# Kernel optimization log

Hardware: AMD Instinct MI355X
Metric: run time of the kernel (lower is better)

Reference implementation:

```python
import jax, jax.numpy as jnp
import numpy as np

SEQ_LEN = 64  # config.SEQ_LEN
T, B, N, D = 256, 128, 4, 2
H_HIS, H_INT = 32, 8


def _uniform(key, shape, k):
    return jax.random.uniform(key, shape, jnp.float32, -k, k)


def setup_inputs() -> dict:
    key = jax.random.key(0)
    ks = jax.random.split(key, 12)
    kh = 1.0 / np.sqrt(H_HIS)
    ki = 1.0 / np.sqrt(H_INT)
    ko = 1.0 / np.sqrt(40)
    return {
        "inputs": jax.random.normal(ks[0], (T, B, N, D), jnp.float32),
        # history LSTM (input 2 -> hidden 32), gate order i,f,g,o like torch
        "Wih_his": _uniform(ks[1], (4 * H_HIS, D), kh),
        "Whh_his": _uniform(ks[2], (4 * H_HIS, H_HIS), kh),
        "bih_his": _uniform(ks[3], (4 * H_HIS,), kh),
        "bhh_his": _uniform(ks[4], (4 * H_HIS,), kh),
        # interaction LSTM (input 2 -> hidden 8)
        "Wih_int": _uniform(ks[5], (4 * H_INT, D), ki),
        "Whh_int": _uniform(ks[6], (4 * H_INT, H_INT), ki),
        "bih_int": _uniform(ks[7], (4 * H_INT,), ki),
        "bhh_int": _uniform(ks[8], (4 * H_INT,), ki),
        # output Linear(40 -> 2)
        "W_out": _uniform(ks[9], (2, H_HIS + H_INT), ko),
        "b_out": _uniform(ks[10], (2,), ko),
    }


def _lstm_windows(x_w, valid, Wih, Whh, bih, bhh):
    """Run an LSTM over L steps for T independent windows at once.
    x_w: [L, Tw, B, d]  inputs per step (leading padding for short windows)
    valid: [L, Tw] bool; while False the state is held at zero, which is
    exactly equivalent to starting the window fresh at its first valid step.
    Returns final hidden state h: [Tw, B, H].
    """
    H = Whh.shape[1]
    Tw, Bb = x_w.shape[1], x_w.shape[2]
    b = bih + bhh

    def step(carry, xs):
        h, c = carry
        x, v = xs
        g = x @ Wih.T + h @ Whh.T + b            # [Tw, B, 4H]
        i, f, gg, o = jnp.split(g, 4, axis=-1)
        c_new = jax.nn.sigmoid(f) * c + jax.nn.sigmoid(i) * jnp.tanh(gg)
        h_new = jax.nn.sigmoid(o) * jnp.tanh(c_new)
        m = v[:, None, None]
        return (jnp.where(m, h_new, 0.0), jnp.where(m, c_new, 0.0)), None

    init = (jnp.zeros((Tw, Bb, H), x_w.dtype), jnp.zeros((Tw, Bb, H), x_w.dtype))
    (h, _), _ = jax.lax.scan(step, init, (x_w, valid))
    return h


def reference(inputs, Wih_his, Whh_his, bih_his, bhh_his,
              Wih_int, Whh_int, bih_int, bhh_int, W_out, b_out):
    Tt, Bb, Nn, Dd = inputs.shape
    L = SEQ_LEN
    # window index for output frame t: frames t-L+1 .. t (clipped; invalid masked)
    t = jnp.arange(Tt)[:, None]
    s = jnp.arange(L)[None, :]
    idx = t - (L - 1) + s                      # [T, L]
    valid = (idx >= 0)
    idx_c = jnp.clip(idx, 0, Tt - 1)
    x_his = inputs[:, :, -1, :][idx_c]         # [T, L, B, d] (ego / last node)
    x_int = inputs[:, :, 0, :][idx_c]          # [T, L, B, d] (interaction node)
    x_his = jnp.transpose(x_his, (1, 0, 2, 3))  # [L, T, B, d]
    x_int = jnp.transpose(x_int, (1, 0, 2, 3))
    v = jnp.transpose(valid)                   # [L, T]

    h_his = _lstm_windows(x_his, v, Wih_his, Whh_his, bih_his, bhh_his)  # [T,B,32]
    h_int = _lstm_windows(x_int, v, Wih_int, Whh_int, bih_int, bhh_int)  # [T,B,8]
    emb = jnp.concatenate([h_his, h_int], axis=-1)                       # [T,B,40]
    return emb @ W_out.T + b_out                                         # [T,B,2]
```

## Files before the change

kernel.cpp:

```cpp
#include <hip/hip_runtime.h>


typedef float v2f __attribute__((ext_vector_type(2)));
typedef float v4f __attribute__((ext_vector_type(4)));
typedef _Float16 h8v __attribute__((ext_vector_type(8)));

static __device__ __forceinline__ float fexp2(float x) {
    return __builtin_amdgcn_exp2f(x);
}
static __device__ __forceinline__ float frcp(float x) {
    return __builtin_amdgcn_rcpf(x);
}
static __device__ __forceinline__ void pk_fma(v2f& d, v2f a, v2f b) {
    asm("v_pk_fma_f32 %0, %1, %2, %0" : "+v"(d) : "v"(a), "v"(b));
}
static __device__ __forceinline__ v2f loh(v4f v) {
    return __builtin_shufflevector(v, v, 0, 1);
}
static __device__ __forceinline__ v2f hih(v4f v) {
    return __builtin_shufflevector(v, v, 2, 3);
}
static __device__ __forceinline__ unsigned short f2h(float f) {
    _Float16 h = (_Float16)f;
    unsigned short u;
    __builtin_memcpy(&u, &h, 2);
    return u;
}

#define LOG2E    1.442695041f
#define TWOLOG2E 2.885390082f

__global__ __launch_bounds__(256) void prep_kernel(
    const float* __restrict__ Wih_his, const float* __restrict__ Whh_his,
    const float* __restrict__ bih_his, const float* __restrict__ bhh_his,
    const float* __restrict__ Wih_int, const float* __restrict__ Whh_int,
    const float* __restrict__ bih_int, const float* __restrict__ bhh_int,
    float* __restrict__ ws)
{
    const int i = blockIdx.x * 256 + threadIdx.x;
    if (i < 4480) {
        if (i < 256) {
            const int r = i >> 1;
            const float s = (r >= 64 && r < 96) ? -TWOLOG2E : -LOG2E;
            ws[i] = Wih_his[i] * s;
        } else if (i < 384) {
            const int r = i - 256;
            const float s = (r >= 64 && r < 96) ? -TWOLOG2E : -LOG2E;
            ws[i] = (bih_his[r] + bhh_his[r]) * s;
        } else {
            const int e = i - 384, r = e >> 5;
            const float s = (r >= 64 && r < 96) ? -TWOLOG2E : -LOG2E;
            ws[i] = Whh_his[e] * s;
        }
    } else if (i < 4544) {
        const int e = i - 4480, r = e >> 1;
        const float s = (r >= 16 && r < 24) ? -TWOLOG2E : -LOG2E;
        ws[i] = Wih_int[e] * s;
    } else if (i < 4576) {
        const int r = i - 4544;
        const float s = (r >= 16 && r < 24) ? -TWOLOG2E : -LOG2E;
        ws[i] = (bih_int[r] + bhh_int[r]) * s;
    } else if (i < 4832) {
        const int e = i - 4576, r = e >> 3;
        const float s = (r >= 16 && r < 24) ? -TWOLOG2E : -LOG2E;
        ws[i] = Whh_int[e] * s;
    } else if (i < 4960) {
        const int p = i - 4832;
        const int T = p >> 4, n = p & 15;
        const int gi = T >> 1, u = 2 * n + (T & 1);
        const int r = gi * 32 + u;
        const float s = (gi == 2) ? -TWOLOG2E : -LOG2E;
        ws[5120 + p] = (bih_his[r] + bhh_his[r]) * s;
    } else if (i < 5216) {
        const int e = i - 4960;
        const int p = e >> 1, comp = e & 1;
        const int T = p >> 4, n = p & 15;
        const int gi = T >> 1, u = 2 * n + (T & 1);
        const int r = gi * 32 + u;
        const float s = (gi == 2) ? -TWOLOG2E : -LOG2E;
        ws[5376 + e] = Wih_his[r * 2 + comp] * s;
    } else if (i < 9312) {
        const int e = i - 5216;
        const int p = e >> 5, k = e & 31;
        const int T = p >> 4, n = p & 15;
        const int gi = T >> 1, u = 2 * n + (T & 1);
        const int r = gi * 32 + u;
        const float s = (gi == 2) ? -TWOLOG2E : -LOG2E;
        reinterpret_cast<unsigned short*>(ws)[11776 + e] =
            f2h(Whh_his[r * 32 + k] * s);
    }
}

__global__ __launch_bounds__(64) void int_kernel(
    const float* __restrict__ inp, const float* __restrict__ ws,
    const float* __restrict__ W_out, float* __restrict__ eInt)
{
    __shared__ __align__(16) float ib[2][8][8];

    const int lane = threadIdx.x;
    const int W    = blockIdx.x;
    const int t    = W >> 4;
    const int g    = lane >> 3;
    const int u    = lane & 7;
    const int b    = ((W & 15) << 3) | g;
    const int nsteps = (t >= 63) ? 64 : (t + 1);
    const int tau0   = (t >= 63) ? (t - 63) : 0;

    v2f wi[4][4], wxi[4];
    float bi[4];
    {
        const v2f* wsWi = reinterpret_cast<const v2f*>(ws + 4576);
        const v2f* wsXi = reinterpret_cast<const v2f*>(ws + 4480);
#pragma unroll
        for (int q = 0; q < 4; ++q) {
            const v2f* row = wsWi + (q * 8 + u) * 4;
#pragma unroll
            for (int k = 0; k < 4; ++k) wi[q][k] = row[k];
            bi[q]  = ws[4544 + q * 8 + u];
            wxi[q] = wsXi[q * 8 + u];
        }
    }

    ib[0][g][u] = 0.f;
    float cc = 0.f, h = 0.f;

    const float* xc = inp + tau0 * 1024 + b * 8;
    float2 xv2 = *reinterpret_cast<const float2*>(xc);
    xc += 1024;

#pragma unroll 1
    for (int s = 0; s < nsteps; ++s) {
        __builtin_amdgcn_wave_barrier();
        asm volatile("s_waitcnt lgkmcnt(0)" ::: "memory");
        __builtin_amdgcn_wave_barrier();

        const int rb = s & 1, wb = rb ^ 1;
        const v4f* ip = reinterpret_cast<const v4f*>(&ib[rb][g][0]);
        const v4f i0 = ip[0], i1 = ip[1];

        float2 nx = {0.f, 0.f};
        if (s + 1 < nsteps) nx = *reinterpret_cast<const float2*>(xc);
        xc += 1024;
        const v2f xv = {xv2.x, xv2.y};

        float a[4];
#pragma unroll
        for (int q = 0; q < 4; ++q) {
            v2f acc = {bi[q], 0.f};
            pk_fma(acc, wxi[q], xv);
            pk_fma(acc, wi[q][0], loh(i0));
            pk_fma(acc, wi[q][1], hih(i0));
            pk_fma(acc, wi[q][2], loh(i1));
            pk_fma(acc, wi[q][3], hih(i1));
            a[q] = acc.x + acc.y;
        }
        const float si = frcp(1.f + fexp2(a[0]));
        const float sf = frcp(1.f + fexp2(a[1]));
        const float tg = fmaf(2.f, frcp(1.f + fexp2(a[2])), -1.f);
        const float so = frcp(1.f + fexp2(a[3]));
        cc = fmaf(sf, cc, si * tg);
        h = so * fmaf(-2.f, frcp(1.f + fexp2(TWOLOG2E * cc)), 1.f);
        ib[wb][g][u] = h;

        xv2 = nx;
    }

    float e0 = W_out[32 + u] * h;
    float e1 = W_out[72 + u] * h;
#pragma unroll
    for (int m = 4; m >= 1; m >>= 1) {
        e0 += __shfl_xor(e0, m);
        e1 += __shfl_xor(e1, m);
    }
    if (u == 0) {
        float2 o; o.x = e0; o.y = e1;
        reinterpret_cast<float2*>(eInt)[t * 128 + b] = o;
    }
}

__global__ __launch_bounds__(64) void his_kernel(
    const float* __restrict__ inp, const float* __restrict__ ws,
    const float* __restrict__ W_out, const float* __restrict__ b_out,
    const float* __restrict__ eInt, float* __restrict__ out)
{
    __shared__ __align__(16) unsigned short hm[2][16][40];

    const int lane = threadIdx.x;
    const int n    = lane & 15;
    const int quad = lane >> 4;
    const int Wd   = blockIdx.x;
    const int t    = Wd >> 3;
    const int bg   = Wd & 7;
    const int nsteps = (t >= 63) ? 64 : (t + 1);
    const int tau0   = (t >= 63) ? (t - 63) : 0;

    h8v Bf[8];
    {
        const h8v* wb = reinterpret_cast<const h8v*>(
            reinterpret_cast<const unsigned short*>(ws) + 11776);
#pragma unroll
        for (int T = 0; T < 8; ++T) Bf[T] = wb[(T * 16 + n) * 4 + quad];
    }
    float cb[8], cw0[8], cw1[8];
#pragma unroll
    for (int T = 0; T < 8; ++T) {
        const int p = T * 16 + n;
        cb[T]  = ws[5120 + p];
        cw0[T] = ws[5376 + 2 * p];
        cw1[T] = ws[5376 + 2 * p + 1];
    }

    const int bbase = bg * 16 + quad * 4;
    const float* xp = inp + tau0 * 1024 + bbase * 8 + 6;
    float2 xc[4];
#pragma unroll
    for (int r = 0; r < 4; ++r)
        xc[r] = *reinterpret_cast<const float2*>(xp + r * 8);
    xp += 1024;

    h8v Af = {};
    float cs[4][2] = {};
    float h0[4] = {}, h1[4] = {};

#pragma unroll 1
    for (int s = 0; s < nsteps; ++s) {
        float2 xn[4];
        if (s + 1 < nsteps) {
#pragma unroll
            for (int r = 0; r < 4; ++r)
                xn[r] = *reinterpret_cast<const float2*>(xp + r * 8);
        } else {
#pragma unroll
            for (int r = 0; r < 4; ++r) xn[r] = make_float2(0.f, 0.f);
        }
        xp += 1024;

        v4f D[8];
#pragma unroll
        for (int T = 0; T < 8; ++T) {
            v4f C;
#pragma unroll
            for (int r = 0; r < 4; ++r)
                C[r] = fmaf(cw1[T], xc[r].y, fmaf(cw0[T], xc[r].x, cb[T]));
            D[T] = __builtin_amdgcn_mfma_f32_16x16x32_f16(Af, Bf[T], C, 0, 0, 0);
        }

#pragma unroll
        for (int r = 0; r < 4; ++r) {
            {
                const float si = frcp(1.f + fexp2(D[0][r]));
                const float sf = frcp(1.f + fexp2(D[2][r]));
                const float tg = fmaf(2.f, frcp(1.f + fexp2(D[4][r])), -1.f);
                const float so = frcp(1.f + fexp2(D[6][r]));
                const float cn = fmaf(sf, cs[r][0], si * tg);
                cs[r][0] = cn;
                h0[r] = so * fmaf(-2.f, frcp(1.f + fexp2(TWOLOG2E * cn)), 1.f);
            }
            {
                const float si = frcp(1.f + fexp2(D[1][r]));
                const float sf = frcp(1.f + fexp2(D[3][r]));
                const float tg = fmaf(2.f, frcp(1.f + fexp2(D[5][r])), -1.f);
                const float so = frcp(1.f + fexp2(D[7][r]));
                const float cn = fmaf(sf, cs[r][1], si * tg);
                cs[r][1] = cn;
                h1[r] = so * fmaf(-2.f, frcp(1.f + fexp2(TWOLOG2E * cn)), 1.f);
            }
        }

        if (s + 1 < nsteps) {
            const int bf = s & 1;
#pragma unroll
            for (int r = 0; r < 4; ++r) {
                const unsigned pk =
                    ((unsigned)f2h(h1[r]) << 16) | f2h(h0[r]);
                *reinterpret_cast<unsigned*>(&hm[bf][quad * 4 + r][2 * n]) = pk;
            }
            __builtin_amdgcn_wave_barrier();
            asm volatile("s_waitcnt lgkmcnt(0)" ::: "memory");
            __builtin_amdgcn_wave_barrier();
            Af = *reinterpret_cast<const h8v*>(&hm[bf][n][quad * 8]);
        }

#pragma unroll
        for (int r = 0; r < 4; ++r) xc[r] = xn[r];
    }

    const float wo0a = W_out[2 * n],      wo0b = W_out[2 * n + 1];
    const float wo1a = W_out[40 + 2 * n], wo1b = W_out[40 + 2 * n + 1];
    float e0[4], e1[4];
#pragma unroll
    for (int r = 0; r < 4; ++r) {
        e0[r] = fmaf(wo0b, h1[r], wo0a * h0[r]);
        e1[r] = fmaf(wo1b, h1[r], wo1a * h0[r]);
#pragma unroll
        for (int m = 1; m <= 8; m <<= 1) {
            e0[r] += __shfl_xor(e0[r], m);
            e1[r] += __shfl_xor(e1[r], m);
        }
    }
    if (n == 0) {
        const float bo0 = b_out[0], bo1 = b_out[1];
#pragma unroll
        for (int r = 0; r < 4; ++r) {
            const int chain = t * 128 + bbase + r;
            const float2 ei = reinterpret_cast<const float2*>(eInt)[chain];
            float2 o;
            o.x = e0[r] + ei.x + bo0;
            o.y = e1[r] + ei.y + bo1;
            reinterpret_cast<float2*>(out)[chain] = o;
        }
    }
}

extern "C" void kernel_launch(void* const* d_in, const int* in_sizes, int n_in,
                              void* d_out, int out_size, void* d_ws, size_t ws_size,
                              hipStream_t stream) {
    const float* inp     = (const float*)d_in[0];
    const float* Wih_his = (const float*)d_in[1];
    const float* Whh_his = (const float*)d_in[2];
    const float* bih_his = (const float*)d_in[3];
    const float* bhh_his = (const float*)d_in[4];
    const float* Wih_int = (const float*)d_in[5];
    const float* Whh_int = (const float*)d_in[6];
    const float* bih_int = (const float*)d_in[7];
    const float* bhh_int = (const float*)d_in[8];
    const float* W_out   = (const float*)d_in[9];
    const float* b_out   = (const float*)d_in[10];
    float* out  = (float*)d_out;
    float* ws   = (float*)d_ws;
    float* eInt = ws + 8192;

    prep_kernel<<<dim3(37), dim3(256), 0, stream>>>(
        Wih_his, Whh_his, bih_his, bhh_his,
        Wih_int, Whh_int, bih_int, bhh_int, ws);

    int_kernel<<<dim3(4096), dim3(64), 0, stream>>>(inp, ws, W_out, eInt);

    his_kernel<<<dim3(2048), dim3(64), 0, stream>>>(
        inp, ws, W_out, b_out, eInt, out);
}
```

Measured before the change: 209.8 us.

## Fuse interaction LSTM into history kernel using MFMA with padded weights

Removes the separate scalar interaction-LSTM kernel and its eInt intermediate, and computes the 8-unit interaction LSTM inside the history kernel. The interaction recurrence now uses two zero-padded 16x16x32 f16 MFMAs per step, with gate exchange done by lane shuffles. The prep kernel writes the reordered f16 interaction weights. This saves a kernel launch and the eInt round trip, and lets the two recurrences overlap in one wave. The cost is extra MFMA and transcendental work on the history kernel's critical path, plus f16 precision for the interaction recurrent weights.

```diff
diff --git a/kernel.cpp b/kernel.cpp
--- a/kernel.cpp
+++ b/kernel.cpp
@@ -1,7 +1,6 @@
 #include <hip/hip_runtime.h>
 
 
-typedef float v2f __attribute__((ext_vector_type(2)));
 typedef float v4f __attribute__((ext_vector_type(4)));
 typedef _Float16 h8v __attribute__((ext_vector_type(8)));
 
@@ -10,15 +9,6 @@
 }
 static __device__ __forceinline__ float frcp(float x) {
     return __builtin_amdgcn_rcpf(x);
-}
-static __device__ __forceinline__ void pk_fma(v2f& d, v2f a, v2f b) {
-    asm("v_pk_fma_f32 %0, %1, %2, %0" : "+v"(d) : "v"(a), "v"(b));
-}
-static __device__ __forceinline__ v2f loh(v4f v) {
-    return __builtin_shufflevector(v, v, 0, 1);
-}
-static __device__ __forceinline__ v2f hih(v4f v) {
-    return __builtin_shufflevector(v, v, 2, 3);
 }
 static __device__ __forceinline__ unsigned short f2h(float f) {
     _Float16 h = (_Float16)f;
@@ -38,152 +28,64 @@
     float* __restrict__ ws)
 {
     const int i = blockIdx.x * 256 + threadIdx.x;
-    if (i < 4480) {
-        if (i < 256) {
-            const int r = i >> 1;
-            const float s = (r >= 64 && r < 96) ? -TWOLOG2E : -LOG2E;
-            ws[i] = Wih_his[i] * s;
-        } else if (i < 384) {
-            const int r = i - 256;
-            const float s = (r >= 64 && r < 96) ? -TWOLOG2E : -LOG2E;
-            ws[i] = (bih_his[r] + bhh_his[r]) * s;
-        } else {
-            const int e = i - 384, r = e >> 5;
-            const float s = (r >= 64 && r < 96) ? -TWOLOG2E : -LOG2E;
-            ws[i] = Whh_his[e] * s;
-        }
-    } else if (i < 4544) {
-        const int e = i - 4480, r = e >> 1;
-        const float s = (r >= 16 && r < 24) ? -TWOLOG2E : -LOG2E;
-        ws[i] = Wih_int[e] * s;
-    } else if (i < 4576) {
-        const int r = i - 4544;
-        const float s = (r >= 16 && r < 24) ? -TWOLOG2E : -LOG2E;
-        ws[i] = (bih_int[r] + bhh_int[r]) * s;
-    } else if (i < 4832) {
-        const int e = i - 4576, r = e >> 3;
-        const float s = (r >= 16 && r < 24) ? -TWOLOG2E : -LOG2E;
-        ws[i] = Whh_int[e] * s;
-    } else if (i < 4960) {
-        const int p = i - 4832;
+    unsigned short* wsu = reinterpret_cast<unsigned short*>(ws);
+    if (i < 128) {
+        const int p = i;
         const int T = p >> 4, n = p & 15;
         const int gi = T >> 1, u = 2 * n + (T & 1);
         const int r = gi * 32 + u;
         const float s = (gi == 2) ? -TWOLOG2E : -LOG2E;
         ws[5120 + p] = (bih_his[r] + bhh_his[r]) * s;
-    } else if (i < 5216) {
-        const int e = i - 4960;
+    } else if (i < 384) {
+        const int e = i - 128;
         const int p = e >> 1, comp = e & 1;
         const int T = p >> 4, n = p & 15;
         const int gi = T >> 1, u = 2 * n + (T & 1);
         const int r = gi * 32 + u;
         const float s = (gi == 2) ? -TWOLOG2E : -LOG2E;
         ws[5376 + e] = Wih_his[r * 2 + comp] * s;
-    } else if (i < 9312) {
-        const int e = i - 5216;
+    } else if (i < 4480) {
+        const int e = i - 384;
         const int p = e >> 5, k = e & 31;
         const int T = p >> 4, n = p & 15;
         const int gi = T >> 1, u = 2 * n + (T & 1);
         const int r = gi * 32 + u;
         const float s = (gi == 2) ? -TWOLOG2E : -LOG2E;
-        reinterpret_cast<unsigned short*>(ws)[11776 + e] =
-            f2h(Whh_his[r * 32 + k] * s);
-    }
-}
-
-__global__ __launch_bounds__(64) void int_kernel(
-    const float* __restrict__ inp, const float* __restrict__ ws,
-    const float* __restrict__ W_out, float* __restrict__ eInt)
-{
-    __shared__ __align__(16) float ib[2][8][8];
-
-    const int lane = threadIdx.x;
-    const int W    = blockIdx.x;
-    const int t    = W >> 4;
-    const int g    = lane >> 3;
-    const int u    = lane & 7;
-    const int b    = ((W & 15) << 3) | g;
-    const int nsteps = (t >= 63) ? 64 : (t + 1);
-    const int tau0   = (t >= 63) ? (t - 63) : 0;
-
-    v2f wi[4][4], wxi[4];
-    float bi[4];
-    {
-        const v2f* wsWi = reinterpret_cast<const v2f*>(ws + 4576);
-        const v2f* wsXi = reinterpret_cast<const v2f*>(ws + 4480);
-#pragma unroll
-        for (int q = 0; q < 4; ++q) {
-            const v2f* row = wsWi + (q * 8 + u) * 4;
-#pragma unroll
-            for (int k = 0; k < 4; ++k) wi[q][k] = row[k];
-            bi[q]  = ws[4544 + q * 8 + u];
-            wxi[q] = wsXi[q * 8 + u];
-        }
-    }
-
-    ib[0][g][u] = 0.f;
-    float cc = 0.f, h = 0.f;
-
-    const float* xc = inp + tau0 * 1024 + b * 8;
-    float2 xv2 = *reinterpret_cast<const float2*>(xc);
-    xc += 1024;
-
-#pragma unroll 1
-    for (int s = 0; s < nsteps; ++s) {
-        __builtin_amdgcn_wave_barrier();
-        asm volatile("s_waitcnt lgkmcnt(0)" ::: "memory");
-        __builtin_amdgcn_wave_barrier();
-
-        const int rb = s & 1, wb = rb ^ 1;
-        const v4f* ip = reinterpret_cast<const v4f*>(&ib[rb][g][0]);
-        const v4f i0 = ip[0], i1 = ip[1];
-
-        float2 nx = {0.f, 0.f};
-        if (s + 1 < nsteps) nx = *reinterpret_cast<const float2*>(xc);
-        xc += 1024;
-        const v2f xv = {xv2.x, xv2.y};
-
-        float a[4];
-#pragma unroll
-        for (int q = 0; q < 4; ++q) {
-            v2f acc = {bi[q], 0.f};
-            pk_fma(acc, wxi[q], xv);
-            pk_fma(acc, wi[q][0], loh(i0));
-            pk_fma(acc, wi[q][1], hih(i0));
-            pk_fma(acc, wi[q][2], loh(i1));
-            pk_fma(acc, wi[q][3], hih(i1));
-            a[q] = acc.x + acc.y;
-        }
-        const float si = frcp(1.f + fexp2(a[0]));
-        const float sf = frcp(1.f + fexp2(a[1]));
-        const float tg = fmaf(2.f, frcp(1.f + fexp2(a[2])), -1.f);
-        const float so = frcp(1.f + fexp2(a[3]));
-        cc = fmaf(sf, cc, si * tg);
-        h = so * fmaf(-2.f, frcp(1.f + fexp2(TWOLOG2E * cc)), 1.f);
-        ib[wb][g][u] = h;
-
-        xv2 = nx;
-    }
-
-    float e0 = W_out[32 + u] * h;
-    float e1 = W_out[72 + u] * h;
-#pragma unroll
-    for (int m = 4; m >= 1; m >>= 1) {
-        e0 += __shfl_xor(e0, m);
-        e1 += __shfl_xor(e1, m);
-    }
-    if (u == 0) {
-        float2 o; o.x = e0; o.y = e1;
-        reinterpret_cast<float2*>(eInt)[t * 128 + b] = o;
-    }
-}
-
-__global__ __launch_bounds__(64) void his_kernel(
+        wsu[11776 + e] = f2h(Whh_his[r * 32 + k] * s);
+    } else if (i < 4512) {
+        const int p2 = i - 4480;
+        const int t = p2 >> 4, n = p2 & 15;
+        const int r2 = (t == 0) ? ((n < 8) ? n : n + 8)
+                                : ((n < 8) ? n + 8 : n + 16);
+        const float s = (r2 >= 16 && r2 < 24) ? -TWOLOG2E : -LOG2E;
+        ws[8192 + p2] = (bih_int[r2] + bhh_int[r2]) * s;
+    } else if (i < 4576) {
+        const int e = i - 4512;
+        const int p2 = e >> 1, comp = e & 1;
+        const int t = p2 >> 4, n = p2 & 15;
+        const int r2 = (t == 0) ? ((n < 8) ? n : n + 8)
+                                : ((n < 8) ? n + 8 : n + 16);
+        const float s = (r2 >= 16 && r2 < 24) ? -TWOLOG2E : -LOG2E;
+        ws[8224 + e] = Wih_int[r2 * 2 + comp] * s;
+    } else if (i < 5600) {
+        const int e = i - 4576;
+        const int p2 = e >> 5, k = e & 31;
+        const int t = p2 >> 4, n = p2 & 15;
+        const int r2 = (t == 0) ? ((n < 8) ? n : n + 8)
+                                : ((n < 8) ? n + 8 : n + 16);
+        const float s = (r2 >= 16 && r2 < 24) ? -TWOLOG2E : -LOG2E;
+        wsu[16640 + e] = (k < 8) ? f2h(Whh_int[r2 * 8 + k] * s)
+                                 : (unsigned short)0;
+    }
+}
+
+__global__ __launch_bounds__(64) void traj_kernel(
     const float* __restrict__ inp, const float* __restrict__ ws,
     const float* __restrict__ W_out, const float* __restrict__ b_out,
-    const float* __restrict__ eInt, float* __restrict__ out)
+    float* __restrict__ out)
 {
     __shared__ __align__(16) unsigned short hm[2][16][40];
+    __shared__ __align__(16) unsigned short hmI[2][16][8];
 
     const int lane = threadIdx.x;
     const int n    = lane & 15;
@@ -193,15 +95,20 @@
     const int bg   = Wd & 7;
     const int nsteps = (t >= 63) ? 64 : (t + 1);
     const int tau0   = (t >= 63) ? (t - 63) : 0;
-
-    h8v Bf[8];
+    const bool lo  = (n < 8);
+
+    h8v Bf[8], BfI[2];
     {
         const h8v* wb = reinterpret_cast<const h8v*>(
             reinterpret_cast<const unsigned short*>(ws) + 11776);
 #pragma unroll
         for (int T = 0; T < 8; ++T) Bf[T] = wb[(T * 16 + n) * 4 + quad];
-    }
-    float cb[8], cw0[8], cw1[8];
+        const h8v* wbI = reinterpret_cast<const h8v*>(
+            reinterpret_cast<const unsigned short*>(ws) + 16640);
+#pragma unroll
+        for (int T = 0; T < 2; ++T) BfI[T] = wbI[(T * 16 + n) * 4 + quad];
+    }
+    float cb[8], cw0[8], cw1[8], cbI[2], cwI0[2], cwI1[2];
 #pragma unroll
     for (int T = 0; T < 8; ++T) {
         const int p = T * 16 + n;
@@ -209,31 +116,45 @@
         cw0[T] = ws[5376 + 2 * p];
         cw1[T] = ws[5376 + 2 * p + 1];
     }
+#pragma unroll
+    for (int T = 0; T < 2; ++T) {
+        const int p2 = T * 16 + n;
+        cbI[T]  = ws[8192 + p2];
+        cwI0[T] = ws[8224 + 2 * p2];
+        cwI1[T] = ws[8224 + 2 * p2 + 1];
+    }
 
     const int bbase = bg * 16 + quad * 4;
-    const float* xp = inp + tau0 * 1024 + bbase * 8 + 6;
-    float2 xc[4];
-#pragma unroll
-    for (int r = 0; r < 4; ++r)
-        xc[r] = *reinterpret_cast<const float2*>(xp + r * 8);
-    xp += 1024;
-
-    h8v Af = {};
-    float cs[4][2] = {};
-    float h0[4] = {}, h1[4] = {};
+    const float* xpB = inp + tau0 * 1024 + bbase * 8;
+    float2 xc[4], xcI[4];
+#pragma unroll
+    for (int r = 0; r < 4; ++r) {
+        xc[r]  = *reinterpret_cast<const float2*>(xpB + r * 8 + 6);
+        xcI[r] = *reinterpret_cast<const float2*>(xpB + r * 8);
+    }
+    xpB += 1024;
+
+    h8v Af = {}, Afi = {};
+    float cs[4][2] = {}, csI[4] = {};
+    float h0[4] = {}, h1[4] = {}, hI[4] = {};
 
 #pragma unroll 1
     for (int s = 0; s < nsteps; ++s) {
-        float2 xn[4];
+        float2 xn[4], xnI[4];
         if (s + 1 < nsteps) {
 #pragma unroll
-            for (int r = 0; r < 4; ++r)
-                xn[r] = *reinterpret_cast<const float2*>(xp + r * 8);
+            for (int r = 0; r < 4; ++r) {
+                xn[r]  = *reinterpret_cast<const float2*>(xpB + r * 8 + 6);
+                xnI[r] = *reinterpret_cast<const float2*>(xpB + r * 8);
+            }
         } else {
 #pragma unroll
-            for (int r = 0; r < 4; ++r) xn[r] = make_float2(0.f, 0.f);
-        }
-        xp += 1024;
+            for (int r = 0; r < 4; ++r) {
+                xn[r] = make_float2(0.f, 0.f);
+                xnI[r] = make_float2(0.f, 0.f);
+            }
+        }
+        xpB += 1024;
 
         v4f D[8];
 #pragma unroll
@@ -243,6 +164,15 @@
             for (int r = 0; r < 4; ++r)
                 C[r] = fmaf(cw1[T], xc[r].y, fmaf(cw0[T], xc[r].x, cb[T]));
             D[T] = __builtin_amdgcn_mfma_f32_16x16x32_f16(Af, Bf[T], C, 0, 0, 0);
+        }
+        v4f DI[2];
+#pragma unroll
+        for (int T = 0; T < 2; ++T) {
+            v4f C;
+#pragma unroll
+            for (int r = 0; r < 4; ++r)
+                C[r] = fmaf(cwI1[T], xcI[r].y, fmaf(cwI0[T], xcI[r].x, cbI[T]));
+            DI[T] = __builtin_amdgcn_mfma_f32_16x16x32_f16(Afi, BfI[T], C, 0, 0, 0);
         }
 
 #pragma unroll
@@ -267,6 +197,22 @@
             }
         }
 
+#pragma unroll
+        for (int r = 0; r < 4; ++r) {
+            const float r0 = frcp(1.f + fexp2(DI[0][r]));
+            const float v0 = lo ? r0 : fmaf(2.f, r0, -1.f);
+            const float v1 = frcp(1.f + fexp2(DI[1][r]));
+            const float o0 = __shfl_xor(v0, 8);
+            const float o1 = __shfl_xor(v1, 8);
+            const float gi = lo ? v0 : o0;
+            const float gf = lo ? v1 : o1;
+            const float gg = lo ? o0 : v0;
+            const float go = lo ? o1 : v1;
+            const float cn = fmaf(gf, csI[r], gi * gg);
+            csI[r] = cn;
+            hI[r] = go * fmaf(-2.f, frcp(1.f + fexp2(TWOLOG2E * cn)), 1.f);
+        }
+
         if (s + 1 < nsteps) {
             const int bf = s & 1;
 #pragma unroll
@@ -275,14 +221,21 @@
                     ((unsigned)f2h(h1[r]) << 16) | f2h(h0[r]);
                 *reinterpret_cast<unsigned*>(&hm[bf][quad * 4 + r][2 * n]) = pk;
             }
+            if (lo) {
+#pragma unroll
+                for (int r = 0; r < 4; ++r)
+                    hmI[bf][quad * 4 + r][n] = f2h(hI[r]);
+            }
             __builtin_amdgcn_wave_barrier();
             asm volatile("s_waitcnt lgkmcnt(0)" ::: "memory");
             __builtin_amdgcn_wave_barrier();
             Af = *reinterpret_cast<const h8v*>(&hm[bf][n][quad * 8]);
-        }
-
-#pragma unroll
-        for (int r = 0; r < 4; ++r) xc[r] = xn[r];
+            if (quad == 0)
+                Afi = *reinterpret_cast<const h8v*>(&hmI[bf][n][0]);
+        }
+
+#pragma unroll
+        for (int r = 0; r < 4; ++r) { xc[r] = xn[r]; xcI[r] = xnI[r]; }
     }
 
     const float wo0a = W_out[2 * n],      wo0b = W_out[2 * n + 1];
@@ -292,6 +245,10 @@
     for (int r = 0; r < 4; ++r) {
         e0[r] = fmaf(wo0b, h1[r], wo0a * h0[r]);
         e1[r] = fmaf(wo1b, h1[r], wo1a * h0[r]);
+        if (lo) {
+            e0[r] = fmaf(W_out[32 + n], hI[r], e0[r]);
+            e1[r] = fmaf(W_out[72 + n], hI[r], e1[r]);
+        }
 #pragma unroll
         for (int m = 1; m <= 8; m <<= 1) {
             e0[r] += __shfl_xor(e0[r], m);
@@ -303,10 +260,9 @@
 #pragma unroll
         for (int r = 0; r < 4; ++r) {
             const int chain = t * 128 + bbase + r;
-            const float2 ei = reinterpret_cast<const float2*>(eInt)[chain];
             float2 o;
-            o.x = e0[r] + ei.x + bo0;
-            o.y = e1[r] + ei.y + bo1;
+            o.x = e0[r] + bo0;
+            o.y = e1[r] + bo1;
             reinterpret_cast<float2*>(out)[chain] = o;
         }
     }
@@ -326,16 +282,13 @@
     const float* bhh_int = (const float*)d_in[8];
     const float* W_out   = (const float*)d_in[9];
     const float* b_out   = (const float*)d_in[10];
-    float* out  = (float*)d_out;
-    float* ws   = (float*)d_ws;
-    float* eInt = ws + 8192;
-
-    prep_kernel<<<dim3(37), dim3(256), 0, stream>>>(
+    float* out = (float*)d_out;
+    float* ws  = (float*)d_ws;
+
+    prep_kernel<<<dim3(22), dim3(256), 0, stream>>>(
         Wih_his, Whh_his, bih_his, bhh_his,
         Wih_int, Whh_int, bih_int, bhh_int, ws);
 
-    int_kernel<<<dim3(4096), dim3(64), 0, stream>>>(inp, ws, W_out, eInt);
-
-    his_kernel<<<dim3(2048), dim3(64), 0, stream>>>(
-        inp, ws, W_out, b_out, eInt, out);
-}
+    traj_kernel<<<dim3(2048), dim3(64), 0, stream>>>(
+        inp, ws, W_out, b_out, out);
+}
```

Result: slower. 235.4 us (+12.2%).
